# Kernel tuning notes

Measured on AMD Instinct MI355X. Metric: run time of the kernel, lower is better.

Reference implementation:

```python
import jax, jax.numpy as jnp
import numpy as np

MAX_W, MIN_W = 120, 24


def setup_inputs() -> dict:
    key = jax.random.key(0)
    ks = jax.random.split(key, 11)
    B, S, D, H = 2, 2048, 1024, 16
    hd = D // H
    s = 1.0 / float(np.sqrt(D))
    return {
        "x": jax.random.normal(ks[0], (B, S, D), jnp.float32),
        "alpha": jnp.float32(0.1),
        "Wq": jax.random.normal(ks[1], (D, D), jnp.float32) * s,
        "bq": jnp.zeros((D,), jnp.float32),
        "Wk": jax.random.normal(ks[2], (D, D), jnp.float32) * s,
        "bk": jnp.zeros((D,), jnp.float32),
        "Wv": jax.random.normal(ks[3], (D, D), jnp.float32) * s,
        "bv": jnp.zeros((D,), jnp.float32),
        "W_o": jax.random.normal(ks[4], (H, hd, hd), jnp.float32),
        "Wfc": jax.random.normal(ks[5], (D, D), jnp.float32) * s,
        "bfc": jnp.zeros((D,), jnp.float32),
    }


def reference(x, alpha, Wq, bq, Wk, bk, Wv, bv, W_o, Wfc, bfc):
    B, S, D = x.shape
    H, hd, _ = W_o.shape
    # --- dynamic window size (step==0 path of the module) ---
    fluct = jnp.abs(x[:, -1] - x[:, -2])            # [B, D]
    a = jax.nn.sigmoid(alpha)
    ewma_prev = fluct[0, 0]                          # step==0: ewma_prev = fluct_step_value
    signal = a * fluct.mean() + (1.0 - a) * ewma_prev
    scale = jax.nn.sigmoid(signal)
    w = jnp.floor(MIN_W + (MAX_W - MIN_W) * scale).astype(jnp.int32)  # int() truncation
    half = w // 2
    # --- projections ---
    q = (x @ Wq + bq).reshape(B, S, H, hd).transpose(0, 2, 1, 3)  # [B,H,S,hd]
    k = (x @ Wk + bk).reshape(B, S, H, hd).transpose(0, 2, 1, 3)
    v = (x @ Wv + bv).reshape(B, S, H, hd).transpose(0, 2, 1, 3)
    inv_sqrt = 1.0 / float(np.sqrt(hd))
    scores = jnp.einsum('bhqd,bhkd->bhqk', q, k) * inv_sqrt       # [B,H,S,S]
    # banded window mask: allowed iff i - w//2 <= j <= i + w//2
    idx = jnp.arange(S)
    band = jnp.abs(idx[:, None] - idx[None, :]) <= half            # [S,S]
    scores = jnp.where(band[None, None], scores, -1e30)
    attn = jax.nn.softmax(scores, axis=-1)
    out = jnp.einsum('bhqk,bhkd->bhqd', attn, v)                   # [B,H,S,hd]
    out = jnp.einsum('bhqd,hdk->bhqk', out, W_o)                   # per-head output matmul
    out = out.transpose(0, 2, 1, 3).reshape(B, S, D)
    return out @ Wfc + bfc
```

## Files before the change

### kernel.cpp

```cpp
#include <hip/hip_runtime.h>
#include <hip/hip_bf16.h>
#include <stdint.h>

#define S_LEN 2048
#define DMODEL 1024
#define NHEAD 16
#define HDIM 64
#define BATCH 2
#define MROWS (BATCH * S_LEN)
#define QKV_LD 3072

typedef unsigned short u16;
typedef __attribute__((ext_vector_type(8))) short bf16x8;
typedef __attribute__((ext_vector_type(4))) float f32x4;

__device__ inline u16 f32_to_bf16(float f) {
  union { float f; unsigned int u; } v; v.f = f;
  unsigned int u = v.u;
  unsigned int r = (u + 0x7fffu + ((u >> 16) & 1u)) >> 16;
  return (u16)r;
}

__device__ inline void gload16(const u16* g, u16* l) {
  __builtin_amdgcn_global_load_lds(
      (const __attribute__((address_space(1))) unsigned int*)g,
      (__attribute__((address_space(3))) unsigned int*)l, 16, 0, 0);
}

__global__ void win_kernel(const float* __restrict__ x, const float* __restrict__ alpha,
                           int* __restrict__ halfw) {
  __shared__ float red[4];
  int tid = threadIdx.x;
  float s = 0.f;
  for (int i = tid; i < BATCH * DMODEL; i += 256) {
    int b = i >> 10, d = i & 1023;
    size_t base = (size_t)b * S_LEN * DMODEL + d;
    float f1 = x[base + (size_t)(S_LEN - 1) * DMODEL];
    float f0 = x[base + (size_t)(S_LEN - 2) * DMODEL];
    s += fabsf(f1 - f0);
  }
#pragma unroll
  for (int m = 32; m >= 1; m >>= 1) s += __shfl_xor(s, m, 64);
  if ((tid & 63) == 0) red[tid >> 6] = s;
  __syncthreads();
  if (tid == 0) {
    float total = red[0] + red[1] + red[2] + red[3];
    float mean = total / (float)(BATCH * DMODEL);
    float e1 = x[(size_t)(S_LEN - 1) * DMODEL];
    float e0 = x[(size_t)(S_LEN - 2) * DMODEL];
    float ew = fabsf(e1 - e0);
    float a = 1.f / (1.f + expf(-alpha[0]));
    float sig = a * mean + (1.f - a) * ew;
    float scale = 1.f / (1.f + expf(-sig));
    int wv = (int)floorf(24.f + 96.f * scale);
    *halfw = wv >> 1;
  }
}

__global__ __launch_bounds__(256) void conv_x_bf16(const float* __restrict__ x,
                                                   u16* __restrict__ xb) {
  size_t i = ((size_t)blockIdx.x * 256 + threadIdx.x) * 8;
  float4 v0 = *(const float4*)(x + i);
  float4 v1 = *(const float4*)(x + i + 4);
  bf16x8 r;
  r[0] = (short)f32_to_bf16(v0.x); r[1] = (short)f32_to_bf16(v0.y);
  r[2] = (short)f32_to_bf16(v0.z); r[3] = (short)f32_to_bf16(v0.w);
  r[4] = (short)f32_to_bf16(v1.x); r[5] = (short)f32_to_bf16(v1.y);
  r[6] = (short)f32_to_bf16(v1.z); r[7] = (short)f32_to_bf16(v1.w);
  *(bf16x8*)(xb + i) = r;
}

__global__ __launch_bounds__(256) void transpose_qkv(const float* __restrict__ Wq,
                                                     const float* __restrict__ Wk,
                                                     const float* __restrict__ Wv,
                                                     u16* __restrict__ Wt) {
  __shared__ float tile[32][33];
  const float* W = blockIdx.z == 0 ? Wq : (blockIdx.z == 1 ? Wk : Wv);
  int k0 = blockIdx.x * 32, n0 = blockIdx.y * 32;
  int tx = threadIdx.x, ty = threadIdx.y;
#pragma unroll
  for (int i = 0; i < 4; ++i)
    tile[ty + i * 8][tx] = W[(size_t)(k0 + ty + i * 8) * DMODEL + n0 + tx];
  __syncthreads();
  u16* o = Wt + (size_t)blockIdx.z * DMODEL * DMODEL;
#pragma unroll
  for (int i = 0; i < 4; ++i)
    o[(size_t)(n0 + ty + i * 8) * DMODEL + k0 + tx] = f32_to_bf16(tile[tx][ty + i * 8]);
}

__global__ __launch_bounds__(128) void build_wc(const float* __restrict__ W_o,
                                                const float* __restrict__ Wfc,
                                                u16* __restrict__ Wc_t) {
  __shared__ float lds[64 * 128];
  int nb = blockIdx.x, h = blockIdx.y, tx = threadIdx.x;
  int n0 = nb * 128;
#pragma unroll
  for (int c = 0; c < 64; ++c)
    lds[c * 128 + tx] = Wfc[(size_t)(h * 64 + c) * DMODEL + n0 + tx];
  __syncthreads();
  float acc[64];
#pragma unroll
  for (int d = 0; d < 64; ++d) acc[d] = 0.f;
  for (int c = 0; c < 64; ++c) {
    float wv = lds[c * 128 + tx];
#pragma unroll
    for (int d = 0; d < 64; ++d)
      acc[d] += W_o[(size_t)(h * 64 + d) * 64 + c] * wv;
  }
  u16 tmp[64];
#pragma unroll
  for (int d = 0; d < 64; ++d) tmp[d] = f32_to_bf16(acc[d]);
  u16* dst = Wc_t + (size_t)(n0 + tx) * DMODEL + h * 64;
#pragma unroll
  for (int q = 0; q < 8; ++q)
    *(bf16x8*)(dst + q * 8) = *(bf16x8*)(tmp + q * 8);
}

#define G1_BM 256
#define G1_BN 192
#define G1_ASZ (G1_BM * 64)
#define G1_BSZ (G1_BN * 64)
__global__ __launch_bounds__(512, 2) void gemm_qkv(
    const u16* __restrict__ A, const u16* __restrict__ Bt,
    const float* __restrict__ bq, const float* __restrict__ bk,
    const float* __restrict__ bv, u16* __restrict__ out) {
  __shared__ __align__(16) u16 smem[2][G1_ASZ + G1_BSZ];

  const int tid = threadIdx.x;
  const int l = tid & 63, w = tid >> 6;
  const int wr = w >> 2, wc = w & 3;
  const int lrow = l & 15, lk = l >> 4;

  const int wgid = (blockIdx.x & 7) * 32 + (blockIdx.x >> 3);
  const int bm = wgid >> 4, bn = wgid & 15;
  const int rowA0 = bm * G1_BM;
  const int colB0 = bn * G1_BN;

  f32x4 acc[8][3] = {};

  auto stage = [&](int buf, int kt) {
    u16* As = smem[buf];
    u16* Bs = smem[buf] + G1_ASZ;
#pragma unroll
    for (int i = 0; i < 4; ++i) {
      int c = i * 512 + tid;
      int row = c >> 3, u = c & 7;
      const u16* g = A + (size_t)(rowA0 + row) * DMODEL + kt + ((u ^ (row & 7)) << 3);
      gload16(g, As + c * 8);
    }
#pragma unroll
    for (int i = 0; i < 3; ++i) {
      int c = i * 512 + tid;
      int row = c >> 3, u = c & 7;
      const u16* g = Bt + (size_t)(colB0 + row) * DMODEL + kt + ((u ^ (row & 7)) << 3);
      gload16(g, Bs + c * 8);
    }
  };

  stage(0, 0);
  asm volatile("s_waitcnt vmcnt(0)");
  __syncthreads();

  int buf = 0;
#pragma unroll 1
  for (int t = 0; t < 16; ++t) {
    if (t < 15) stage(buf ^ 1, (t + 1) * 64);
    const u16* As = smem[buf];
    const u16* Bs = smem[buf] + G1_ASZ;
#pragma unroll
    for (int kk = 0; kk < 2; ++kk) {
      bf16x8 af[8], bg[3];
      const int ksw = ((kk << 2) + lk);
#pragma unroll
      for (int m = 0; m < 8; ++m) {
        int r = wr * 128 + m * 16 + lrow;
        af[m] = *(const bf16x8*)(As + r * 64 + ((ksw ^ (lrow & 7)) << 3));
      }
#pragma unroll
      for (int n = 0; n < 3; ++n) {
        int r = wc * 48 + n * 16 + lrow;
        bg[n] = *(const bf16x8*)(Bs + r * 64 + ((ksw ^ (lrow & 7)) << 3));
      }
#pragma unroll
      for (int m = 0; m < 8; ++m)
#pragma unroll
        for (int n = 0; n < 3; ++n)
          acc[m][n] = __builtin_amdgcn_mfma_f32_16x16x32_bf16(af[m], bg[n], acc[m][n], 0, 0, 0);
    }
    if (t < 15) {
      asm volatile("s_waitcnt vmcnt(0)");
      __syncthreads();
      buf ^= 1;
    }
  }

#pragma unroll
  for (int n = 0; n < 3; ++n) {
    int c = colB0 + wc * 48 + n * 16 + lrow;
    float bias = (c < 1024) ? bq[c] : ((c < 2048) ? bk[c - 1024] : bv[c - 2048]);
    float mult = (c < 1024) ? 0.125f : 1.0f;
#pragma unroll
    for (int m = 0; m < 8; ++m) {
      int r0 = rowA0 + wr * 128 + m * 16 + lk * 4;
#pragma unroll
      for (int j = 0; j < 4; ++j)
        out[(size_t)(r0 + j) * QKV_LD + c] = f32_to_bf16((acc[m][n][j] + bias) * mult);
    }
  }
}

template <int BF16_OUT>
__global__ __launch_bounds__(256) void gemm_bt(
    const u16* __restrict__ A, const u16* __restrict__ Bt,
    const float* __restrict__ bias0, const float* __restrict__ bias1,
    const float* __restrict__ bias2,
    void* __restrict__ out0, void* __restrict__ out1, void* __restrict__ out2,
    int K) {
  __shared__ __align__(16) u16 smem[128 * 64 * 2];
  u16* As = smem;
  u16* Bs = smem + 128 * 64;

  const int tid = threadIdx.x;
  const int l = tid & 63, w = tid >> 6;
  const int wr = w >> 1, wc = w & 1;
  const int lrow = l & 15, lk = l >> 4;
  const int bm = blockIdx.x, bn = blockIdx.y;
  const int rowA0 = bm * 128, rowB0 = bn * 128;

  f32x4 acc[4][4] = {};

  for (int kt = 0; kt < K; kt += 64) {
    __syncthreads();
#pragma unroll
    for (int i = 0; i < 4; ++i) {
      int c_lin = i * 256 + tid;
      int row = c_lin >> 3, u = c_lin & 7;
      const u16* g = A + (size_t)(rowA0 + row) * K + kt + ((u ^ (row & 7)) << 3);
      gload16(g, As + (i * 2048 + w * 512));
    }
#pragma unroll
    for (int i = 0; i < 4; ++i) {
      int c_lin = i * 256 + tid;
      int row = c_lin >> 3, u = c_lin & 7;
      const u16* g = Bt + (size_t)(rowB0 + row) * K + kt + ((u ^ (row & 7)) << 3);
      gload16(g, Bs + (i * 2048 + w * 512));
    }
    asm volatile("s_waitcnt vmcnt(0)");
    __syncthreads();
#pragma unroll
    for (int kk = 0; kk < 2; ++kk) {
      bf16x8 af[4], bg[4];
#pragma unroll
      for (int m = 0; m < 4; ++m) {
        int r = wr * 64 + m * 16 + lrow;
        af[m] = *(const bf16x8*)(As + r * 64 + ((((kk << 2) + lk) ^ (lrow & 7)) << 3));
      }
#pragma unroll
      for (int n = 0; n < 4; ++n) {
        int r = wc * 64 + n * 16 + lrow;
        bg[n] = *(const bf16x8*)(Bs + r * 64 + ((((kk << 2) + lk) ^ (lrow & 7)) << 3));
      }
#pragma unroll
      for (int m = 0; m < 4; ++m)
#pragma unroll
        for (int n = 0; n < 4; ++n)
          acc[m][n] = __builtin_amdgcn_mfma_f32_16x16x32_bf16(af[m], bg[n], acc[m][n], 0, 0, 0);
    }
  }

  const int sub = rowB0 >> 10;
  const float* bias = sub == 0 ? bias0 : (sub == 1 ? bias1 : bias2);
  void* outp = sub == 0 ? out0 : (sub == 1 ? out1 : out2);
  const int orow0 = rowA0 + wr * 64;
  const int ocol0 = (rowB0 & 1023) + wc * 64;
#pragma unroll
  for (int m = 0; m < 4; ++m)
#pragma unroll
    for (int n = 0; n < 4; ++n) {
      int c = ocol0 + n * 16 + lrow;
      float bv = bias[c];
#pragma unroll
      for (int j = 0; j < 4; ++j) {
        int r = orow0 + m * 16 + lk * 4 + j;
        float v = acc[m][n][j] + bv;
        if (BF16_OUT)
          ((u16*)outp)[(size_t)r * DMODEL + c] = f32_to_bf16(v);
        else
          ((float*)outp)[(size_t)r * DMODEL + c] = v;
      }
    }
}

__global__ __launch_bounds__(256) void attn_win(const u16* __restrict__ qkv,
                                                u16* __restrict__ ao,
                                                const int* __restrict__ halfptr) {
  __shared__ __align__(16) u16 KsPs[192 * 72];
  __shared__ __align__(16) u16 Vt[64 * 200];
  const int tid = threadIdx.x, l = tid & 63, w = tid >> 6;
  const int lrow = l & 15, lk = l >> 4;
  const int qb_i = blockIdx.x, h = blockIdx.y, b = blockIdx.z;
  const int q0 = qb_i * 64, k0 = q0 - 64;
  const int halfw = *halfptr;

  const u16* qb = qkv;
  const u16* kb = qkv + 1024;
  const u16* vb = qkv + 2048;

  const bf16x8 zero = {0, 0, 0, 0, 0, 0, 0, 0};
#pragma unroll
  for (int i = 0; i < 6; ++i) {
    int c = i * 256 + tid;
    int row = c >> 3, ch = c & 7;
    int key = k0 + row;
    bf16x8 v = zero;
    if (key >= 0 && key < S_LEN)
      v = *(const bf16x8*)(kb + (size_t)(b * S_LEN + key) * QKV_LD + h * 64 + ch * 8);
    *(bf16x8*)(KsPs + row * 72 + ch * 8) = v;
  }
#pragma unroll
  for (int i = 0; i < 6; ++i) {
    int c = i * 256 + tid;
    int row = c % 192, ch = c / 192;
    int key = k0 + row;
    bf16x8 v = zero;
    if (key >= 0 && key < S_LEN)
      v = *(const bf16x8*)(vb + (size_t)(b * S_LEN + key) * QKV_LD + h * 64 + ch * 8);
#pragma unroll
    for (int e = 0; e < 8; ++e)
      Vt[(ch * 8 + e) * 200 + row] = (u16)v[e];
  }
  const int qrow = q0 + w * 16 + lrow;
  bf16x8 qf[2];
#pragma unroll
  for (int kk = 0; kk < 2; ++kk)
    qf[kk] = *(const bf16x8*)(qb + (size_t)(b * S_LEN + qrow) * QKV_LD + h * 64 + kk * 32 + lk * 8);

  __syncthreads();

  f32x4 sc[12];
#pragma unroll
  for (int f = 0; f < 12; ++f) sc[f] = (f32x4){0.f, 0.f, 0.f, 0.f};
#pragma unroll
  for (int kk = 0; kk < 2; ++kk) {
#pragma unroll
    for (int f = 0; f < 12; ++f) {
      bf16x8 kf = *(const bf16x8*)(KsPs + (f * 16 + lrow) * 72 + kk * 32 + lk * 8);
      sc[f] = __builtin_amdgcn_mfma_f32_16x16x32_bf16(qf[kk], kf, sc[f], 0, 0, 0);
    }
  }
  float rmax[4] = {-3e38f, -3e38f, -3e38f, -3e38f};
  const int qbase = q0 + w * 16 + lk * 4;
#pragma unroll
  for (int f = 0; f < 12; ++f) {
    int kj = k0 + f * 16 + lrow;
    bool kok = (kj >= 0) && (kj < S_LEN);
#pragma unroll
    for (int j = 0; j < 4; ++j) {
      int qi = qbase + j;
      float v = sc[f][j];
      int dd = qi - kj;
      int ad = dd < 0 ? -dd : dd;
      v = (kok && ad <= halfw) ? v : -1e30f;
      sc[f][j] = v;
      rmax[j] = fmaxf(rmax[j], v);
    }
  }
#pragma unroll
  for (int j = 0; j < 4; ++j) {
    rmax[j] = fmaxf(rmax[j], __shfl_xor(rmax[j], 1, 16));
    rmax[j] = fmaxf(rmax[j], __shfl_xor(rmax[j], 2, 16));
    rmax[j] = fmaxf(rmax[j], __shfl_xor(rmax[j], 4, 16));
    rmax[j] = fmaxf(rmax[j], __shfl_xor(rmax[j], 8, 16));
  }
  float rsum[4] = {0.f, 0.f, 0.f, 0.f};
#pragma unroll
  for (int f = 0; f < 12; ++f)
#pragma unroll
    for (int j = 0; j < 4; ++j) {
      float e = __expf(sc[f][j] - rmax[j]);
      sc[f][j] = e;
      rsum[j] += e;
    }
#pragma unroll
  for (int j = 0; j < 4; ++j) {
    rsum[j] += __shfl_xor(rsum[j], 1, 16);
    rsum[j] += __shfl_xor(rsum[j], 2, 16);
    rsum[j] += __shfl_xor(rsum[j], 4, 16);
    rsum[j] += __shfl_xor(rsum[j], 8, 16);
  }
  float rinv[4];
#pragma unroll
  for (int j = 0; j < 4; ++j) rinv[j] = 1.0f / rsum[j];

  __syncthreads();

  u16* Ps = KsPs;
#pragma unroll
  for (int f = 0; f < 12; ++f)
#pragma unroll
    for (int j = 0; j < 4; ++j) {
      int prow = w * 16 + lk * 4 + j;
      Ps[prow * 200 + f * 16 + lrow] = f32_to_bf16(sc[f][j] * rinv[j]);
    }
  __syncthreads();

  f32x4 o[4] = {};
#pragma unroll
  for (int jt = 0; jt < 6; ++jt) {
    bf16x8 pa = *(const bf16x8*)(Ps + (w * 16 + lrow) * 200 + jt * 32 + lk * 8);
#pragma unroll
    for (int n = 0; n < 4; ++n) {
      bf16x8 vf = *(const bf16x8*)(Vt + (n * 16 + lrow) * 200 + jt * 32 + lk * 8);
      o[n] = __builtin_amdgcn_mfma_f32_16x16x32_bf16(pa, vf, o[n], 0, 0, 0);
    }
  }
#pragma unroll
  for (int n = 0; n < 4; ++n)
#pragma unroll
    for (int j = 0; j < 4; ++j) {
      int qi = q0 + w * 16 + lk * 4 + j;
      int d = n * 16 + lrow;
      ao[(size_t)(b * S_LEN + qi) * DMODEL + h * 64 + d] = f32_to_bf16(o[n][j]);
    }
}

extern "C" void kernel_launch(void* const* d_in, const int* in_sizes, int n_in,
                              void* d_out, int out_size, void* d_ws, size_t ws_size,
                              hipStream_t stream) {
  (void)in_sizes; (void)n_in; (void)out_size; (void)ws_size;
  const float* x     = (const float*)d_in[0];
  const float* alpha = (const float*)d_in[1];
  const float* Wq    = (const float*)d_in[2];
  const float* bq    = (const float*)d_in[3];
  const float* Wk    = (const float*)d_in[4];
  const float* bk    = (const float*)d_in[5];
  const float* Wv    = (const float*)d_in[6];
  const float* bv    = (const float*)d_in[7];
  const float* W_o   = (const float*)d_in[8];
  const float* Wfc   = (const float*)d_in[9];
  const float* bfc   = (const float*)d_in[10];

  char* ws = (char*)d_ws;
  int* halfw  = (int*)ws;
  u16* xb     = (u16*)(ws + 256);
  u16* Wqkv_t = xb + (size_t)MROWS * DMODEL;
  u16* qkv    = Wqkv_t + (size_t)3 * DMODEL * DMODEL;
  u16* ao     = qkv + (size_t)MROWS * QKV_LD;
  u16* Wc_t   = ao + (size_t)MROWS * DMODEL;

  hipLaunchKernelGGL(win_kernel, dim3(1), dim3(256), 0, stream, x, alpha, halfw);
  hipLaunchKernelGGL(conv_x_bf16, dim3(MROWS * DMODEL / (256 * 8)), dim3(256), 0, stream, x, xb);
  hipLaunchKernelGGL(transpose_qkv, dim3(32, 32, 3), dim3(32, 8), 0, stream, Wq, Wk, Wv, Wqkv_t);
  hipLaunchKernelGGL(build_wc, dim3(8, 16), dim3(128), 0, stream, W_o, Wfc, Wc_t);
  hipLaunchKernelGGL(gemm_qkv, dim3(256), dim3(512), 0, stream,
                     xb, Wqkv_t, bq, bk, bv, qkv);
  hipLaunchKernelGGL(attn_win, dim3(S_LEN / 64, NHEAD, BATCH), dim3(256), 0, stream,
                     qkv, ao, halfw);
  hipLaunchKernelGGL((gemm_bt<0>), dim3(32, 8), dim3(256), 0, stream,
                     ao, Wc_t, bfc, bfc, bfc, d_out, d_out, d_out, DMODEL);
}
```

Before: 118.2 us.

## Fuse window kernel, double-buffer FC GEMM, async K loads, remap QKV tiles

Folds the window-size reduction into an extra block of the bf16 conversion kernel, removing one launch. Replaces the generic FC GEMM with a double-buffered version that prefetches the next K tile while computing the current one. Changes the QKV GEMM tile-to-XCD mapping so each XCD shares column tiles. In attention, K is loaded asynchronously into swizzled LDS, V is staged through registers so its transpose overlaps the QK MFMAs, and the bounds checks are dropped. Without those checks, out-of-range keys read neighbouring workspace memory and depend on the band mask to hide it.

Result: faster. 104.5 us (-11.6%).

```diff
diff --git a/kernel.cpp b/kernel.cpp
--- a/kernel.cpp
+++ b/kernel.cpp
@@ -1,6 +1,7 @@
 #include <hip/hip_runtime.h>
 #include <hip/hip_bf16.h>
 #include <stdint.h>
+#include <stddef.h>
 
 #define S_LEN 2048
 #define DMODEL 1024
@@ -27,38 +28,39 @@
       (__attribute__((address_space(3))) unsigned int*)l, 16, 0, 0);
 }
 
-__global__ void win_kernel(const float* __restrict__ x, const float* __restrict__ alpha,
-                           int* __restrict__ halfw) {
-  __shared__ float red[4];
-  int tid = threadIdx.x;
-  float s = 0.f;
-  for (int i = tid; i < BATCH * DMODEL; i += 256) {
-    int b = i >> 10, d = i & 1023;
-    size_t base = (size_t)b * S_LEN * DMODEL + d;
-    float f1 = x[base + (size_t)(S_LEN - 1) * DMODEL];
-    float f0 = x[base + (size_t)(S_LEN - 2) * DMODEL];
-    s += fabsf(f1 - f0);
-  }
-#pragma unroll
-  for (int m = 32; m >= 1; m >>= 1) s += __shfl_xor(s, m, 64);
-  if ((tid & 63) == 0) red[tid >> 6] = s;
-  __syncthreads();
-  if (tid == 0) {
-    float total = red[0] + red[1] + red[2] + red[3];
-    float mean = total / (float)(BATCH * DMODEL);
-    float e1 = x[(size_t)(S_LEN - 1) * DMODEL];
-    float e0 = x[(size_t)(S_LEN - 2) * DMODEL];
-    float ew = fabsf(e1 - e0);
-    float a = 1.f / (1.f + expf(-alpha[0]));
-    float sig = a * mean + (1.f - a) * ew;
-    float scale = 1.f / (1.f + expf(-sig));
-    int wv = (int)floorf(24.f + 96.f * scale);
-    *halfw = wv >> 1;
-  }
-}
-
 __global__ __launch_bounds__(256) void conv_x_bf16(const float* __restrict__ x,
-                                                   u16* __restrict__ xb) {
+                                                   u16* __restrict__ xb,
+                                                   const float* __restrict__ alpha,
+                                                   int* __restrict__ halfw) {
+  if (blockIdx.x == 2048) {
+    __shared__ float red[4];
+    int tid = threadIdx.x;
+    float s = 0.f;
+    for (int i = tid; i < BATCH * DMODEL; i += 256) {
+      int b = i >> 10, d = i & 1023;
+      size_t base = (size_t)b * S_LEN * DMODEL + d;
+      float f1 = x[base + (size_t)(S_LEN - 1) * DMODEL];
+      float f0 = x[base + (size_t)(S_LEN - 2) * DMODEL];
+      s += fabsf(f1 - f0);
+    }
+#pragma unroll
+    for (int m = 32; m >= 1; m >>= 1) s += __shfl_xor(s, m, 64);
+    if ((tid & 63) == 0) red[tid >> 6] = s;
+    __syncthreads();
+    if (tid == 0) {
+      float total = red[0] + red[1] + red[2] + red[3];
+      float mean = total / (float)(BATCH * DMODEL);
+      float e1 = x[(size_t)(S_LEN - 1) * DMODEL];
+      float e0 = x[(size_t)(S_LEN - 2) * DMODEL];
+      float ew = fabsf(e1 - e0);
+      float a = 1.f / (1.f + expf(-alpha[0]));
+      float sig = a * mean + (1.f - a) * ew;
+      float scale = 1.f / (1.f + expf(-sig));
+      int wv = (int)floorf(24.f + 96.f * scale);
+      *halfw = wv >> 1;
+    }
+    return;
+  }
   size_t i = ((size_t)blockIdx.x * 256 + threadIdx.x) * 8;
   float4 v0 = *(const float4*)(x + i);
   float4 v1 = *(const float4*)(x + i + 4);
@@ -131,8 +133,10 @@
   const int wr = w >> 2, wc = w & 3;
   const int lrow = l & 15, lk = l >> 4;
 
-  const int wgid = (blockIdx.x & 7) * 32 + (blockIdx.x >> 3);
-  const int bm = wgid >> 4, bn = wgid & 15;
+  const int xcd = blockIdx.x & 7;
+  const int idx = blockIdx.x >> 3;
+  const int bm = idx & 15;
+  const int bn = xcd * 2 + (idx >> 4);
   const int rowA0 = bm * G1_BM;
   const int colB0 = bn * G1_BN;
 
@@ -209,56 +213,65 @@
   }
 }
 
-template <int BF16_OUT>
-__global__ __launch_bounds__(256) void gemm_bt(
-    const u16* __restrict__ A, const u16* __restrict__ Bt,
-    const float* __restrict__ bias0, const float* __restrict__ bias1,
-    const float* __restrict__ bias2,
-    void* __restrict__ out0, void* __restrict__ out1, void* __restrict__ out2,
-    int K) {
-  __shared__ __align__(16) u16 smem[128 * 64 * 2];
-  u16* As = smem;
-  u16* Bs = smem + 128 * 64;
+__global__ __launch_bounds__(256) void gemm_fc(const u16* __restrict__ A,
+                                               const u16* __restrict__ Bt,
+                                               const float* __restrict__ bias,
+                                               float* __restrict__ out) {
+  __shared__ __align__(16) u16 smem[2][256 * 64];
 
   const int tid = threadIdx.x;
   const int l = tid & 63, w = tid >> 6;
   const int wr = w >> 1, wc = w & 1;
   const int lrow = l & 15, lk = l >> 4;
-  const int bm = blockIdx.x, bn = blockIdx.y;
-  const int rowA0 = bm * 128, rowB0 = bn * 128;
+
+  const int bn = blockIdx.x & 7;
+  const int bm = blockIdx.x >> 3;
+  const int rowA0 = bm * 128, colB0 = bn * 128;
 
   f32x4 acc[4][4] = {};
 
-  for (int kt = 0; kt < K; kt += 64) {
-    __syncthreads();
+  auto stage = [&](int buf, int kt) {
+    u16* As = smem[buf];
+    u16* Bs = smem[buf] + 128 * 64;
 #pragma unroll
     for (int i = 0; i < 4; ++i) {
-      int c_lin = i * 256 + tid;
-      int row = c_lin >> 3, u = c_lin & 7;
-      const u16* g = A + (size_t)(rowA0 + row) * K + kt + ((u ^ (row & 7)) << 3);
-      gload16(g, As + (i * 2048 + w * 512));
+      int c = i * 256 + tid;
+      int row = c >> 3, u = c & 7;
+      const u16* g = A + (size_t)(rowA0 + row) * DMODEL + kt + ((u ^ (row & 7)) << 3);
+      gload16(g, As + c * 8);
     }
 #pragma unroll
     for (int i = 0; i < 4; ++i) {
-      int c_lin = i * 256 + tid;
-      int row = c_lin >> 3, u = c_lin & 7;
-      const u16* g = Bt + (size_t)(rowB0 + row) * K + kt + ((u ^ (row & 7)) << 3);
-      gload16(g, Bs + (i * 2048 + w * 512));
-    }
-    asm volatile("s_waitcnt vmcnt(0)");
-    __syncthreads();
+      int c = i * 256 + tid;
+      int row = c >> 3, u = c & 7;
+      const u16* g = Bt + (size_t)(colB0 + row) * DMODEL + kt + ((u ^ (row & 7)) << 3);
+      gload16(g, Bs + c * 8);
+    }
+  };
+
+  stage(0, 0);
+  asm volatile("s_waitcnt vmcnt(0)");
+  __syncthreads();
+
+  int buf = 0;
+#pragma unroll 1
+  for (int t = 0; t < 16; ++t) {
+    if (t < 15) stage(buf ^ 1, (t + 1) * 64);
+    const u16* As = smem[buf];
+    const u16* Bs = smem[buf] + 128 * 64;
 #pragma unroll
     for (int kk = 0; kk < 2; ++kk) {
       bf16x8 af[4], bg[4];
+      const int ksw = ((kk << 2) + lk);
 #pragma unroll
       for (int m = 0; m < 4; ++m) {
         int r = wr * 64 + m * 16 + lrow;
-        af[m] = *(const bf16x8*)(As + r * 64 + ((((kk << 2) + lk) ^ (lrow & 7)) << 3));
+        af[m] = *(const bf16x8*)(As + r * 64 + ((ksw ^ (lrow & 7)) << 3));
       }
 #pragma unroll
       for (int n = 0; n < 4; ++n) {
         int r = wc * 64 + n * 16 + lrow;
-        bg[n] = *(const bf16x8*)(Bs + r * 64 + ((((kk << 2) + lk) ^ (lrow & 7)) << 3));
+        bg[n] = *(const bf16x8*)(Bs + r * 64 + ((ksw ^ (lrow & 7)) << 3));
       }
 #pragma unroll
       for (int m = 0; m < 4; ++m)
@@ -266,88 +279,86 @@
         for (int n = 0; n < 4; ++n)
           acc[m][n] = __builtin_amdgcn_mfma_f32_16x16x32_bf16(af[m], bg[n], acc[m][n], 0, 0, 0);
     }
-  }
-
-  const int sub = rowB0 >> 10;
-  const float* bias = sub == 0 ? bias0 : (sub == 1 ? bias1 : bias2);
-  void* outp = sub == 0 ? out0 : (sub == 1 ? out1 : out2);
-  const int orow0 = rowA0 + wr * 64;
-  const int ocol0 = (rowB0 & 1023) + wc * 64;
-#pragma unroll
-  for (int m = 0; m < 4; ++m)
-#pragma unroll
-    for (int n = 0; n < 4; ++n) {
-      int c = ocol0 + n * 16 + lrow;
-      float bv = bias[c];
-#pragma unroll
-      for (int j = 0; j < 4; ++j) {
-        int r = orow0 + m * 16 + lk * 4 + j;
-        float v = acc[m][n][j] + bv;
-        if (BF16_OUT)
-          ((u16*)outp)[(size_t)r * DMODEL + c] = f32_to_bf16(v);
-        else
-          ((float*)outp)[(size_t)r * DMODEL + c] = v;
-      }
-    }
+    if (t < 15) {
+      asm volatile("s_waitcnt vmcnt(0)");
+      __syncthreads();
+      buf ^= 1;
+    }
+  }
+
+#pragma unroll
+  for (int n = 0; n < 4; ++n) {
+    int c = colB0 + wc * 64 + n * 16 + lrow;
+    float bv = bias[c];
+#pragma unroll
+    for (int m = 0; m < 4; ++m) {
+      int r0 = rowA0 + wr * 64 + m * 16 + lk * 4;
+#pragma unroll
+      for (int j = 0; j < 4; ++j)
+        out[(size_t)(r0 + j) * DMODEL + c] = acc[m][n][j] + bv;
+    }
+  }
 }
 
 __global__ __launch_bounds__(256) void attn_win(const u16* __restrict__ qkv,
                                                 u16* __restrict__ ao,
                                                 const int* __restrict__ halfptr) {
-  __shared__ __align__(16) u16 KsPs[192 * 72];
+  __shared__ __align__(16) u16 KP[12800];
   __shared__ __align__(16) u16 Vt[64 * 200];
   const int tid = threadIdx.x, l = tid & 63, w = tid >> 6;
   const int lrow = l & 15, lk = l >> 4;
-  const int qb_i = blockIdx.x, h = blockIdx.y, b = blockIdx.z;
-  const int q0 = qb_i * 64, k0 = q0 - 64;
+  const int q0 = blockIdx.x * 64, k0 = q0 - 64;
+  const int h = blockIdx.y, b = blockIdx.z;
   const int halfw = *halfptr;
 
   const u16* qb = qkv;
   const u16* kb = qkv + 1024;
   const u16* vb = qkv + 2048;
 
-  const bf16x8 zero = {0, 0, 0, 0, 0, 0, 0, 0};
 #pragma unroll
   for (int i = 0; i < 6; ++i) {
     int c = i * 256 + tid;
-    int row = c >> 3, ch = c & 7;
-    int key = k0 + row;
-    bf16x8 v = zero;
-    if (key >= 0 && key < S_LEN)
-      v = *(const bf16x8*)(kb + (size_t)(b * S_LEN + key) * QKV_LD + h * 64 + ch * 8);
-    *(bf16x8*)(KsPs + row * 72 + ch * 8) = v;
-  }
+    int row = c >> 3, u = c & 7;
+    const u16* g = kb + (ptrdiff_t)((b * S_LEN + k0 + row) * QKV_LD + h * 64 + ((u ^ (row & 7)) << 3));
+    gload16(g, KP + c * 8);
+  }
+  const int qrow = q0 + w * 16 + lrow;
+  bf16x8 qf[2];
+#pragma unroll
+  for (int kk = 0; kk < 2; ++kk)
+    qf[kk] = *(const bf16x8*)(qb + (ptrdiff_t)((b * S_LEN + qrow) * QKV_LD + h * 64 + kk * 32 + lk * 8));
+  bf16x8 vreg[6];
 #pragma unroll
   for (int i = 0; i < 6; ++i) {
     int c = i * 256 + tid;
     int row = c % 192, ch = c / 192;
-    int key = k0 + row;
-    bf16x8 v = zero;
-    if (key >= 0 && key < S_LEN)
-      v = *(const bf16x8*)(vb + (size_t)(b * S_LEN + key) * QKV_LD + h * 64 + ch * 8);
+    vreg[i] = *(const bf16x8*)(vb + (ptrdiff_t)((b * S_LEN + k0 + row) * QKV_LD + h * 64 + ch * 8));
+  }
+
+  asm volatile("s_waitcnt vmcnt(0)" ::: "memory");
+  __syncthreads();
+
+  f32x4 sc[12];
+#pragma unroll
+  for (int f = 0; f < 12; ++f) sc[f] = (f32x4){0.f, 0.f, 0.f, 0.f};
+#pragma unroll
+  for (int kk = 0; kk < 2; ++kk) {
+#pragma unroll
+    for (int f = 0; f < 12; ++f) {
+      bf16x8 kf = *(const bf16x8*)(KP + (f * 16 + lrow) * 64 + ((((kk << 2) + lk) ^ (lrow & 7)) << 3));
+      sc[f] = __builtin_amdgcn_mfma_f32_16x16x32_bf16(qf[kk], kf, sc[f], 0, 0, 0);
+    }
+  }
+
+#pragma unroll
+  for (int i = 0; i < 6; ++i) {
+    int c = i * 256 + tid;
+    int row = c % 192, ch = c / 192;
 #pragma unroll
     for (int e = 0; e < 8; ++e)
-      Vt[(ch * 8 + e) * 200 + row] = (u16)v[e];
-  }
-  const int qrow = q0 + w * 16 + lrow;
-  bf16x8 qf[2];
-#pragma unroll
-  for (int kk = 0; kk < 2; ++kk)
-    qf[kk] = *(const bf16x8*)(qb + (size_t)(b * S_LEN + qrow) * QKV_LD + h * 64 + kk * 32 + lk * 8);
-
-  __syncthreads();
-
-  f32x4 sc[12];
-#pragma unroll
-  for (int f = 0; f < 12; ++f) sc[f] = (f32x4){0.f, 0.f, 0.f, 0.f};
-#pragma unroll
-  for (int kk = 0; kk < 2; ++kk) {
-#pragma unroll
-    for (int f = 0; f < 12; ++f) {
-      bf16x8 kf = *(const bf16x8*)(KsPs + (f * 16 + lrow) * 72 + kk * 32 + lk * 8);
-      sc[f] = __builtin_amdgcn_mfma_f32_16x16x32_bf16(qf[kk], kf, sc[f], 0, 0, 0);
-    }
-  }
+      Vt[(ch * 8 + e) * 200 + row] = (u16)vreg[i][e];
+  }
+
   float rmax[4] = {-3e38f, -3e38f, -3e38f, -3e38f};
   const int qbase = q0 + w * 16 + lk * 4;
 #pragma unroll
@@ -394,7 +405,7 @@
 
   __syncthreads();
 
-  u16* Ps = KsPs;
+  u16* Ps = KP;
 #pragma unroll
   for (int f = 0; f < 12; ++f)
 #pragma unroll
@@ -448,14 +459,14 @@
   u16* ao     = qkv + (size_t)MROWS * QKV_LD;
   u16* Wc_t   = ao + (size_t)MROWS * DMODEL;
 
-  hipLaunchKernelGGL(win_kernel, dim3(1), dim3(256), 0, stream, x, alpha, halfw);
-  hipLaunchKernelGGL(conv_x_bf16, dim3(MROWS * DMODEL / (256 * 8)), dim3(256), 0, stream, x, xb);
+  hipLaunchKernelGGL(conv_x_bf16, dim3(MROWS * DMODEL / (256 * 8) + 1), dim3(256), 0, stream,
+                     x, xb, alpha, halfw);
   hipLaunchKernelGGL(transpose_qkv, dim3(32, 32, 3), dim3(32, 8), 0, stream, Wq, Wk, Wv, Wqkv_t);
   hipLaunchKernelGGL(build_wc, dim3(8, 16), dim3(128), 0, stream, W_o, Wfc, Wc_t);
   hipLaunchKernelGGL(gemm_qkv, dim3(256), dim3(512), 0, stream,
                      xb, Wqkv_t, bq, bk, bv, qkv);
   hipLaunchKernelGGL(attn_win, dim3(S_LEN / 64, NHEAD, BATCH), dim3(256), 0, stream,
                      qkv, ao, halfw);
-  hipLaunchKernelGGL((gemm_bt<0>), dim3(32, 8), dim3(256), 0, stream,
-                     ao, Wc_t, bfc, bfc, bfc, d_out, d_out, d_out, DMODEL);
-}
+  hipLaunchKernelGGL(gemm_fc, dim3(256), dim3(256), 0, stream,
+                     ao, Wc_t, bfc, (float*)d_out);
+}
```
